# Performance work log

Hardware: AMD Instinct MI355X
Metric: run time of the kernel (lower is better)

Reference implementation:

```python
import jax, jax.numpy as jnp
import numpy as np

VERY_NEG = -1e30

H = 768           # hidden_size
A_DIM = 768       # attention_dim_size
N_TREE = 40000    # num_tree_nodes (embed_init vocab)
N_CODES = 10000   # number of leaf codes (rows of leaves_list)
MAX_ANC = 8       # max ancestors per code
B, V, M = 16, 32, 48  # batch, visits, codes per visit
OUT = 512         # classifier output_size


def setup_inputs() -> dict:
    key = jax.random.key(0)
    ks = jax.random.split(key, 12)
    leaves_list = jax.random.randint(ks[0], (N_CODES, MAX_ANC), 0, N_TREE)
    ancestors_list = jax.random.randint(ks[1], (N_CODES, MAX_ANC), 0, N_TREE)
    masks = (jax.random.uniform(ks[2], (N_CODES, MAX_ANC)) > 0.3).astype(jnp.float32)
    masks = masks.at[:, 0].set(1.0)  # ensure at least one valid ancestor
    input_ids = jax.random.randint(ks[3], (B, V, M), 0, N_CODES + 1)  # 0 is padding row
    code_mask = (jax.random.uniform(ks[4], (B, V, M)) > 0.2).astype(jnp.float32)
    code_mask = code_mask.at[:, :, 0].set(1.0)
    s = 1.0 / np.sqrt(H)
    embed_table = jax.random.normal(ks[5], (N_TREE, H), dtype=jnp.float32) * s
    w1 = jax.random.normal(ks[6], (2 * H, A_DIM), dtype=jnp.float32) * (1.0 / np.sqrt(2 * H))
    b1 = jnp.zeros((A_DIM,), dtype=jnp.float32)
    w2 = jax.random.normal(ks[7], (A_DIM, 1), dtype=jnp.float32) * (1.0 / np.sqrt(A_DIM))
    b2 = jnp.zeros((1,), dtype=jnp.float32)
    wc = jax.random.normal(ks[8], (H, OUT), dtype=jnp.float32) * s
    bc = jnp.zeros((OUT,), dtype=jnp.float32)
    return {
        "embed_table": embed_table, "w1": w1, "b1": b1, "w2": w2, "b2": b2,
        "wc": wc, "bc": bc, "masks": masks, "code_mask": code_mask,
        "leaves_list": leaves_list, "ancestors_list": ancestors_list,
        "input_ids": input_ids,
    }


def reference(embed_table, w1, b1, w2, b2, wc, bc, masks, code_mask,
              leaves_list, ancestors_list, input_ids):
    # --- DAGAttention2D over ancestor axis ---
    leaves = embed_table[leaves_list]        # [N, A, H]
    ancestors = embed_table[ancestors_list]  # [N, A, H]
    m = masks[:, :, None]                    # [N, A, 1]
    x = jnp.concatenate([leaves * m, ancestors * m], axis=-1)  # [N, A, 2H]
    x = jax.nn.relu(jnp.einsum('nah,hd->nad', x, w1) + b1)
    x = jnp.einsum('nad,do->nao', x, w2) + b2                  # [N, A, 1]
    x = x + (1.0 - m) * VERY_NEG
    attn = jax.nn.softmax(x, axis=1)                           # softmax over ancestors
    dag_emb = (attn * ancestors * m).sum(axis=1)               # [N, H]
    # --- dict_matrix with padding row 0, embedding lookup ---
    dict_matrix = jnp.concatenate([jnp.zeros((1, dag_emb.shape[1]), dag_emb.dtype), dag_emb], axis=0)
    emb = dict_matrix[input_ids]             # [B, V, M, H]
    cm = code_mask[..., None]
    pooled = (emb * cm).sum(axis=2) / jnp.clip(cm.sum(axis=2), 1.0, None)  # [B, V, H]
    # --- Classifier (dropout inactive at eval, activation=None) ---
    out = jnp.einsum('bvh,ho->bvo', pooled, wc) + bc           # [B, V, OUT]
    return out
```

## Files before the change

kernel.cpp:

```cpp
#include <hip/hip_runtime.h>
#include <stdint.h>

typedef unsigned short u16;
typedef __bf16 bfx8 __attribute__((ext_vector_type(8)));
typedef float f32x4 __attribute__((ext_vector_type(4)));

#define HD 768
#define NTREE 40000
#define NCODES 10000
#define GNN 1536
#define OUTD 512
#define NBV 512
#define VNEG (-1e30f)
#define TB 4

#define BM 256
#define BN 256
#define BK 64
#define NKT (HD / BK)
#define NMT ((NTREE + BM - 1) / BM)
#define NNT (GNN / BN)
#define GRID (NMT * NNT)
#define Q8 (GRID / 8)
#define R8 (GRID % 8)

#define WAITV(n) asm volatile("s_waitcnt vmcnt(" #n ")" ::: "memory")

__device__ __forceinline__ float bf2f(u16 u) {
  union { uint32_t i; float f; } v; v.i = ((uint32_t)u) << 16; return v.f;
}
__device__ __forceinline__ u16 f2bf(float f) {
  union { float fl; uint32_t i; } v; v.fl = f;
  uint32_t u = v.i;
  u += 0x7FFFu + ((u >> 16) & 1u);
  return (u16)(u >> 16);
}

__global__ void k_convE(const float* __restrict__ E, u16* __restrict__ Ebf, int n4) {
  int i = blockIdx.x * blockDim.x + threadIdx.x;
  if (i >= n4) return;
  float4 v = ((const float4*)E)[i];
  ushort4 r;
  r.x = f2bf(v.x); r.y = f2bf(v.y); r.z = f2bf(v.z); r.w = f2bf(v.w);
  ((ushort4*)Ebf)[i] = r;
}

__global__ void k_bt(const float* __restrict__ w1, u16* __restrict__ Bt) {
  int idx = blockIdx.x * blockDim.x + threadIdx.x;
  if (idx >= GNN * HD) return;
  int n = idx / HD, k = idx % HD;
  int srow = k + ((n >= HD) ? HD : 0);
  int scol = (n >= HD) ? (n - HD) : n;
  Bt[idx] = f2bf(w1[(size_t)srow * HD + scol]);
}

__global__ __launch_bounds__(512, 2) void k_gemm(const u16* __restrict__ A,
                                                 const u16* __restrict__ B,
                                                 u16* __restrict__ C) {
  __shared__ u16 lds[65536];

  const int tid    = threadIdx.x;
  const int lane   = tid & 63;
  const int wn     = tid >> 6;
  const int lane15 = lane & 15;
  const int g      = lane >> 4;

  const int orig = blockIdx.x;
  const int xcd = orig & 7, lin = orig >> 3;
  const int wg = (xcd < R8 ? xcd * (Q8 + 1) : R8 * (Q8 + 1) + (xcd - R8) * Q8) + lin;
  const int mt = wg / NNT, nt = wg % NNT;
  const int tm = mt * BM, tn = nt * BN;

  const u16* aSrc[2][2];
  const u16* bSrc[2][2];
#pragma unroll
  for (int u = 0; u < 2; ++u) {
    const int o    = u * 8192 + tid * 16;
    const int rloc = o >> 7;
    const int c    = ((o >> 4) & 7) ^ (rloc & 7);
#pragma unroll
    for (int h = 0; h < 2; ++h) {
      int ra = tm + h * 128 + rloc; if (ra > NTREE - 1) ra = NTREE - 1;
      aSrc[u][h] = A + (size_t)ra * HD + c * 8;
      bSrc[u][h] = B + (size_t)(tn + h * 128 + rloc) * HD + c * 8;
    }
  }

#define STAGE_A(MH, NB, TT) do {                                               \
    _Pragma("unroll") for (int u = 0; u < 2; ++u)                              \
      __builtin_amdgcn_global_load_lds(                                        \
        (const __attribute__((address_space(1))) void*)(aSrc[u][MH] + (TT) * BK), \
        (__attribute__((address_space(3))) void*)((char*)lds + (NB) * 32768 +  \
            (MH) * 16384 + u * 8192 + tid * 16),                               \
        16, 0, 0);                                                             \
  } while (0)

#define STAGE_B(NH, NB, TT) do {                                               \
    _Pragma("unroll") for (int u = 0; u < 2; ++u)                              \
      __builtin_amdgcn_global_load_lds(                                        \
        (const __attribute__((address_space(1))) void*)(bSrc[u][NH] + (TT) * BK), \
        (__attribute__((address_space(3))) void*)((char*)lds + 65536 +         \
            (NB) * 32768 + (NH) * 16384 + u * 8192 + tid * 16),                \
        16, 0, 0);                                                             \
  } while (0)

  f32x4 acc[16][2];
#pragma unroll
  for (int i = 0; i < 16; ++i) {
    acc[i][0] = (f32x4){0.f, 0.f, 0.f, 0.f};
    acc[i][1] = (f32x4){0.f, 0.f, 0.f, 0.f};
  }

  int colz[2];
  colz[0] = ((0 * 4 + g) ^ (lane15 & 7)) * 8;
  colz[1] = ((1 * 4 + g) ^ (lane15 & 7)) * 8;
  const int rbase = lane15 * 64;

  bfx8 aF[8], bF[2][2];

#define PHASE(MH, KS, STAGE_STMT, DRAIN_STMT)                                  \
  {                                                                            \
    const int _az = bA + (MH) * 8192 + rbase + colz[KS];                       \
    _Pragma("unroll") for (int i = 0; i < 8; ++i)                              \
      aF[i] = *(const bfx8*)&lds[_az + i * 1024];                              \
    if ((MH) == 0) {                                                           \
      const int _bz = bB + wn * 2048 + rbase + colz[KS];                       \
      bF[KS][0] = *(const bfx8*)&lds[_bz];                                     \
      bF[KS][1] = *(const bfx8*)&lds[_bz + 1024];                              \
    }                                                                          \
    STAGE_STMT;                                                                \
    __builtin_amdgcn_s_barrier();                                              \
    asm volatile("s_waitcnt lgkmcnt(0)" ::: "memory");                         \
    __builtin_amdgcn_sched_barrier(0);                                         \
    __builtin_amdgcn_s_setprio(1);                                             \
    _Pragma("unroll") for (int i = 0; i < 8; ++i) {                            \
      acc[(MH) * 8 + i][0] = __builtin_amdgcn_mfma_f32_16x16x32_bf16(          \
          aF[i], bF[KS][0], acc[(MH) * 8 + i][0], 0, 0, 0);                    \
      acc[(MH) * 8 + i][1] = __builtin_amdgcn_mfma_f32_16x16x32_bf16(          \
          aF[i], bF[KS][1], acc[(MH) * 8 + i][1], 0, 0, 0);                    \
    }                                                                          \
    __builtin_amdgcn_s_setprio(0);                                             \
    DRAIN_STMT;                                                                \
    __builtin_amdgcn_s_barrier();                                              \
  }

  STAGE_B(0, 0, 0);
  STAGE_B(1, 0, 0);
  STAGE_A(0, 0, 0);
  STAGE_A(1, 0, 0);
  WAITV(2);
  __builtin_amdgcn_s_barrier();

  for (int t = 0; t < NKT; ++t) {
    const int cur = t & 1, nb = cur ^ 1;
    const int bA = cur * 16384;
    const int bB = 32768 + cur * 16384;
    const bool more = (t + 1 < NKT);

    PHASE(0, 0, if (more) STAGE_B(0, nb, t + 1), );
    PHASE(0, 1, if (more) STAGE_B(1, nb, t + 1),
          if (t == NKT - 1) { WAITV(0); } else { WAITV(4); });
    PHASE(1, 0, if (more) STAGE_A(0, nb, t + 1), );
    PHASE(1, 1, if (more) STAGE_A(1, nb, t + 1), WAITV(2));
  }

  const int r0 = (lane >> 4) * 4, cc = lane15;
#pragma unroll
  for (int mf = 0; mf < 16; ++mf) {
#pragma unroll
    for (int j = 0; j < 2; ++j) {
#pragma unroll
      for (int rr = 0; rr < 4; ++rr) {
        const int row = tm + mf * 16 + r0 + rr;
        if (row < NTREE) {
          const int col = tn + wn * 32 + j * 16 + cc;
          C[(size_t)row * GNN + col] = f2bf(acc[mf][j][rr]);
        }
      }
    }
  }
#undef PHASE
#undef STAGE_A
#undef STAGE_B
}

__global__ __launch_bounds__(256) void k_attn(const u16* __restrict__ PQ,
                                              const u16* __restrict__ Ebf,
                                              const float* __restrict__ b1,
                                              const float* __restrict__ w2,
                                              const float* __restrict__ b2,
                                              const float* __restrict__ masks,
                                              const int* __restrict__ leaves,
                                              const int* __restrict__ anc,
                                              float* __restrict__ dag) {
  const int n = blockIdx.x;
  const int tid = threadIdx.x, lane = tid & 63, wv = tid >> 6;
  __shared__ float sc[8];
  __shared__ float m_s[8];
  __shared__ int   an_s[8];
  __shared__ int   lv_s[8];
  if (tid < 8) {
    an_s[tid] = anc[n * 8 + tid];
    lv_s[tid] = leaves[n * 8 + tid];
    m_s[tid]  = masks[n * 8 + tid];
  }
  __syncthreads();

  for (int a = wv; a < 8; a += 4) {
    const float mm = m_s[a];
    if (mm == 0.f) {
      if (lane == 0) sc[a] = VNEG;
      continue;
    }
    const int l = lv_s[a], an = an_s[a];
    const u16* pr = PQ + (size_t)l * GNN;
    const u16* qr = PQ + (size_t)an * GNN + HD;
    const int d0 = lane * 12;
    float s = 0.f;
#pragma unroll
    for (int jj = 0; jj < 3; ++jj) {
      const int d = d0 + jj * 4;
      ushort4 pv = *(const ushort4*)(pr + d);
      ushort4 qv = *(const ushort4*)(qr + d);
      float4  bb = *(const float4*)(b1 + d);
      float4  ww = *(const float4*)(w2 + d);
      float v;
      v = fmaxf(bf2f(pv.x) + bf2f(qv.x) + bb.x, 0.f); s += v * ww.x;
      v = fmaxf(bf2f(pv.y) + bf2f(qv.y) + bb.y, 0.f); s += v * ww.y;
      v = fmaxf(bf2f(pv.z) + bf2f(qv.z) + bb.z, 0.f); s += v * ww.z;
      v = fmaxf(bf2f(pv.w) + bf2f(qv.w) + bb.w, 0.f); s += v * ww.w;
    }
#pragma unroll
    for (int off = 32; off > 0; off >>= 1) s += __shfl_down(s, off);
    if (lane == 0) sc[a] = s + b2[0];
  }
  __syncthreads();

  float mx = sc[0];
#pragma unroll
  for (int a = 1; a < 8; ++a) mx = fmaxf(mx, sc[a]);
  float ex[8], den = 0.f;
#pragma unroll
  for (int a = 0; a < 8; ++a) { ex[a] = expf(sc[a] - mx); den += ex[a]; }
  const float inv = 1.0f / den;
  float cf[8];
#pragma unroll
  for (int a = 0; a < 8; ++a) cf[a] = ex[a] * inv * m_s[a];

#pragma unroll
  for (int c = 0; c < 3; ++c) {
    const int d = tid + c * 256;
    float accv = 0.f;
#pragma unroll
    for (int a = 0; a < 8; ++a) {
      const float cfa = cf[a];
      if (cfa != 0.f) accv += cfa * bf2f(Ebf[(size_t)an_s[a] * HD + d]);
    }
    dag[(size_t)n * HD + d] = accv;
  }
}

__global__ __launch_bounds__(256) void k_pool(const float* __restrict__ dag,
                                              const int* __restrict__ ids,
                                              const float* __restrict__ cm,
                                              float* __restrict__ pooled) {
  const int bv = blockIdx.x, tid = threadIdx.x;
  __shared__ int   id_s[48];
  __shared__ float cm_s[48];
  if (tid < 48) { id_s[tid] = ids[bv * 48 + tid]; cm_s[tid] = cm[bv * 48 + tid]; }
  __syncthreads();
  float cnt = 0.f;
  for (int m = 0; m < 48; ++m) cnt += cm_s[m];
  const float scale = 1.0f / fmaxf(cnt, 1.0f);
#pragma unroll
  for (int c = 0; c < 3; ++c) {
    const int d = tid + c * 256;
    float accv = 0.f;
    for (int m = 0; m < 48; ++m) {
      const int id = id_s[m];
      const float cv = cm_s[m];
      if (id > 0 && cv != 0.f) accv += cv * dag[(size_t)(id - 1) * HD + d];
    }
    pooled[(size_t)bv * HD + d] = accv * scale;
  }
}

__global__ __launch_bounds__(256) void k_out(const float* __restrict__ pooled,
                                             const float* __restrict__ wc,
                                             const float* __restrict__ bc,
                                             float* __restrict__ out) {
  const int b0 = blockIdx.x * TB;
  const int tid = threadIdx.x;
  __shared__ float pl[TB][HD];
  for (int i = tid; i < TB * HD; i += 256) pl[i / HD][i % HD] = pooled[(size_t)b0 * HD + i];
  __syncthreads();
  float a0[TB], a1[TB];
#pragma unroll
  for (int r = 0; r < TB; ++r) { a0[r] = 0.f; a1[r] = 0.f; }
  for (int h = 0; h < HD; ++h) {
    const float w0  = wc[(size_t)h * OUTD + tid];
    const float w1v = wc[(size_t)h * OUTD + tid + 256];
#pragma unroll
    for (int r = 0; r < TB; ++r) { const float p = pl[r][h]; a0[r] += p * w0; a1[r] += p * w1v; }
  }
  const float bc0 = bc[tid], bc1 = bc[tid + 256];
#pragma unroll
  for (int r = 0; r < TB; ++r) {
    out[(size_t)(b0 + r) * OUTD + tid]       = a0[r] + bc0;
    out[(size_t)(b0 + r) * OUTD + tid + 256] = a1[r] + bc1;
  }
}

extern "C" void kernel_launch(void* const* d_in, const int* in_sizes, int n_in,
                              void* d_out, int out_size, void* d_ws, size_t ws_size,
                              hipStream_t stream) {
  const float* E     = (const float*)d_in[0];
  const float* w1    = (const float*)d_in[1];
  const float* b1    = (const float*)d_in[2];
  const float* w2    = (const float*)d_in[3];
  const float* b2    = (const float*)d_in[4];
  const float* wc    = (const float*)d_in[5];
  const float* bc    = (const float*)d_in[6];
  const float* masks = (const float*)d_in[7];
  const float* cm    = (const float*)d_in[8];
  const int*   leaves = (const int*)d_in[9];
  const int*   anc    = (const int*)d_in[10];
  const int*   ids    = (const int*)d_in[11];
  float* out = (float*)d_out;

  if (n_in < 12) return;
  if (in_sizes[0] != NTREE * HD) return;
  if (out_size != NBV * OUTD) return;

  char* ws = (char*)d_ws;
  const size_t szEbf = (size_t)NTREE * HD * 2;
  const size_t szBt  = (size_t)GNN * HD * 2;
  const size_t szPQ  = (size_t)NTREE * GNN * 2;
  const size_t szDag = (size_t)NCODES * HD * 4;
  const size_t szPl  = (size_t)NBV * HD * 4;
  if (ws_size < szEbf + szBt + szPQ + szDag + szPl) return;

  u16*   Ebf    = (u16*)ws;            ws += szEbf;
  u16*   Bt     = (u16*)ws;            ws += szBt;
  u16*   PQ     = (u16*)ws;            ws += szPQ;
  float* dag    = (float*)ws;          ws += szDag;
  float* pooled = (float*)ws;          ws += szPl;

  const int n4 = NTREE * HD / 4;
  k_convE<<<(n4 + 255) / 256, 256, 0, stream>>>(E, Ebf, n4);
  k_bt<<<(GNN * HD + 255) / 256, 256, 0, stream>>>(w1, Bt);
  k_gemm<<<GRID, 512, 0, stream>>>(Ebf, Bt, PQ);
  k_attn<<<NCODES, 256, 0, stream>>>(PQ, Ebf, b1, w2, b2, masks, leaves, anc, dag);
  k_pool<<<NBV, 256, 0, stream>>>(dag, ids, cm, pooled);
  k_out<<<NBV / TB, 256, 0, stream>>>(pooled, wc, bc, out);
}
```

Baseline: 316.0 us.

## Use 2x4 warp tiling in GEMM, widen attention blocks, vectorize pooling

```diff
diff --git a/kernel.cpp b/kernel.cpp
--- a/kernel.cpp
+++ b/kernel.cpp
@@ -4,6 +4,7 @@
 typedef unsigned short u16;
 typedef __bf16 bfx8 __attribute__((ext_vector_type(8)));
 typedef float f32x4 __attribute__((ext_vector_type(4)));
+typedef u16 u16x8 __attribute__((ext_vector_type(8)));
 
 #define HD 768
 #define NTREE 40000
@@ -61,7 +62,9 @@
 
   const int tid    = threadIdx.x;
   const int lane   = tid & 63;
-  const int wn     = tid >> 6;
+  const int wv     = tid >> 6;
+  const int wm     = wv >> 2;
+  const int wn2    = wv & 3;
   const int lane15 = lane & 15;
   const int g      = lane >> 4;
 
@@ -104,51 +107,49 @@
         16, 0, 0);                                                             \
   } while (0)
 
-  f32x4 acc[16][2];
-#pragma unroll
-  for (int i = 0; i < 16; ++i) {
-    acc[i][0] = (f32x4){0.f, 0.f, 0.f, 0.f};
-    acc[i][1] = (f32x4){0.f, 0.f, 0.f, 0.f};
-  }
+  f32x4 acc[8][4];
+#pragma unroll
+  for (int i = 0; i < 8; ++i)
+#pragma unroll
+    for (int j = 0; j < 4; ++j) acc[i][j] = (f32x4){0.f, 0.f, 0.f, 0.f};
 
   int colz[2];
   colz[0] = ((0 * 4 + g) ^ (lane15 & 7)) * 8;
   colz[1] = ((1 * 4 + g) ^ (lane15 & 7)) * 8;
-  const int rbase = lane15 * 64;
-
-  bfx8 aF[8], bF[2][2];
+  const int aBase = (wm * 128 + lane15) * 64;
+  const int bBase = (wn2 * 64 + lane15) * 64;
+
+  bfx8 aF[4], bF[4];
 
 #define PHASE(MH, KS, STAGE_STMT, DRAIN_STMT)                                  \
   {                                                                            \
-    const int _az = bA + (MH) * 8192 + rbase + colz[KS];                       \
-    _Pragma("unroll") for (int i = 0; i < 8; ++i)                              \
+    const int _az = bA + aBase + (MH) * 4096 + colz[KS];                       \
+    _Pragma("unroll") for (int i = 0; i < 4; ++i)                              \
       aF[i] = *(const bfx8*)&lds[_az + i * 1024];                              \
     if ((MH) == 0) {                                                           \
-      const int _bz = bB + wn * 2048 + rbase + colz[KS];                       \
-      bF[KS][0] = *(const bfx8*)&lds[_bz];                                     \
-      bF[KS][1] = *(const bfx8*)&lds[_bz + 1024];                              \
+      const int _bz = bB + bBase + colz[KS];                                   \
+      _Pragma("unroll") for (int j = 0; j < 4; ++j)                            \
+        bF[j] = *(const bfx8*)&lds[_bz + j * 1024];                            \
     }                                                                          \
     STAGE_STMT;                                                                \
     __builtin_amdgcn_s_barrier();                                              \
     asm volatile("s_waitcnt lgkmcnt(0)" ::: "memory");                         \
     __builtin_amdgcn_sched_barrier(0);                                         \
     __builtin_amdgcn_s_setprio(1);                                             \
-    _Pragma("unroll") for (int i = 0; i < 8; ++i) {                            \
-      acc[(MH) * 8 + i][0] = __builtin_amdgcn_mfma_f32_16x16x32_bf16(          \
-          aF[i], bF[KS][0], acc[(MH) * 8 + i][0], 0, 0, 0);                    \
-      acc[(MH) * 8 + i][1] = __builtin_amdgcn_mfma_f32_16x16x32_bf16(          \
-          aF[i], bF[KS][1], acc[(MH) * 8 + i][1], 0, 0, 0);                    \
-    }                                                                          \
+    _Pragma("unroll") for (int i = 0; i < 4; ++i)                              \
+      _Pragma("unroll") for (int j = 0; j < 4; ++j)                            \
+        acc[(MH) * 4 + i][j] = __builtin_amdgcn_mfma_f32_16x16x32_bf16(        \
+            aF[i], bF[j], acc[(MH) * 4 + i][j], 0, 0, 0);                      \
     __builtin_amdgcn_s_setprio(0);                                             \
     DRAIN_STMT;                                                                \
     __builtin_amdgcn_s_barrier();                                              \
   }
 
+  STAGE_A(0, 0, 0);
+  STAGE_A(1, 0, 0);
   STAGE_B(0, 0, 0);
   STAGE_B(1, 0, 0);
-  STAGE_A(0, 0, 0);
-  STAGE_A(1, 0, 0);
-  WAITV(2);
+  WAITV(0);
   __builtin_amdgcn_s_barrier();
 
   for (int t = 0; t < NKT; ++t) {
@@ -157,24 +158,23 @@
     const int bB = 32768 + cur * 16384;
     const bool more = (t + 1 < NKT);
 
-    PHASE(0, 0, if (more) STAGE_B(0, nb, t + 1), );
-    PHASE(0, 1, if (more) STAGE_B(1, nb, t + 1),
-          if (t == NKT - 1) { WAITV(0); } else { WAITV(4); });
-    PHASE(1, 0, if (more) STAGE_A(0, nb, t + 1), );
-    PHASE(1, 1, if (more) STAGE_A(1, nb, t + 1), WAITV(2));
+    PHASE(0, 0, if (more) { STAGE_A(0, nb, t + 1); STAGE_A(1, nb, t + 1); }, );
+    PHASE(1, 0, if (more) { STAGE_B(0, nb, t + 1); STAGE_B(1, nb, t + 1); }, );
+    PHASE(0, 1, , );
+    PHASE(1, 1, , WAITV(0));
   }
 
   const int r0 = (lane >> 4) * 4, cc = lane15;
 #pragma unroll
-  for (int mf = 0; mf < 16; ++mf) {
-#pragma unroll
-    for (int j = 0; j < 2; ++j) {
+  for (int mf = 0; mf < 8; ++mf) {
+#pragma unroll
+    for (int nf = 0; nf < 4; ++nf) {
 #pragma unroll
       for (int rr = 0; rr < 4; ++rr) {
-        const int row = tm + mf * 16 + r0 + rr;
+        const int row = tm + wm * 128 + mf * 16 + r0 + rr;
         if (row < NTREE) {
-          const int col = tn + wn * 32 + j * 16 + cc;
-          C[(size_t)row * GNN + col] = f2bf(acc[mf][j][rr]);
+          const int col = tn + wn2 * 64 + nf * 16 + cc;
+          C[(size_t)row * GNN + col] = f2bf(acc[mf][nf][rr]);
         }
       }
     }
@@ -184,7 +184,27 @@
 #undef STAGE_B
 }
 
-__global__ __launch_bounds__(256) void k_attn(const u16* __restrict__ PQ,
+__device__ __forceinline__ float dot8(const u16* pr, const u16* qr,
+                                      const float* b1, const float* w2, int d) {
+  u16x8 pv = *(const u16x8*)(pr + d);
+  u16x8 qv = *(const u16x8*)(qr + d);
+  float4 bb0 = *(const float4*)(b1 + d);
+  float4 bb1 = *(const float4*)(b1 + d + 4);
+  float4 ww0 = *(const float4*)(w2 + d);
+  float4 ww1 = *(const float4*)(w2 + d + 4);
+  float s = 0.f, v;
+  v = fmaxf(bf2f(pv[0]) + bf2f(qv[0]) + bb0.x, 0.f); s += v * ww0.x;
+  v = fmaxf(bf2f(pv[1]) + bf2f(qv[1]) + bb0.y, 0.f); s += v * ww0.y;
+  v = fmaxf(bf2f(pv[2]) + bf2f(qv[2]) + bb0.z, 0.f); s += v * ww0.z;
+  v = fmaxf(bf2f(pv[3]) + bf2f(qv[3]) + bb0.w, 0.f); s += v * ww0.w;
+  v = fmaxf(bf2f(pv[4]) + bf2f(qv[4]) + bb1.x, 0.f); s += v * ww1.x;
+  v = fmaxf(bf2f(pv[5]) + bf2f(qv[5]) + bb1.y, 0.f); s += v * ww1.y;
+  v = fmaxf(bf2f(pv[6]) + bf2f(qv[6]) + bb1.z, 0.f); s += v * ww1.z;
+  v = fmaxf(bf2f(pv[7]) + bf2f(qv[7]) + bb1.w, 0.f); s += v * ww1.w;
+  return s;
+}
+
+__global__ __launch_bounds__(512) void k_attn(const u16* __restrict__ PQ,
                                               const u16* __restrict__ Ebf,
                                               const float* __restrict__ b1,
                                               const float* __restrict__ w2,
@@ -206,33 +226,21 @@
   }
   __syncthreads();
 
-  for (int a = wv; a < 8; a += 4) {
+  {
+    const int a = wv;
     const float mm = m_s[a];
     if (mm == 0.f) {
       if (lane == 0) sc[a] = VNEG;
-      continue;
-    }
-    const int l = lv_s[a], an = an_s[a];
-    const u16* pr = PQ + (size_t)l * GNN;
-    const u16* qr = PQ + (size_t)an * GNN + HD;
-    const int d0 = lane * 12;
-    float s = 0.f;
-#pragma unroll
-    for (int jj = 0; jj < 3; ++jj) {
-      const int d = d0 + jj * 4;
-      ushort4 pv = *(const ushort4*)(pr + d);
-      ushort4 qv = *(const ushort4*)(qr + d);
-      float4  bb = *(const float4*)(b1 + d);
-      float4  ww = *(const float4*)(w2 + d);
-      float v;
-      v = fmaxf(bf2f(pv.x) + bf2f(qv.x) + bb.x, 0.f); s += v * ww.x;
-      v = fmaxf(bf2f(pv.y) + bf2f(qv.y) + bb.y, 0.f); s += v * ww.y;
-      v = fmaxf(bf2f(pv.z) + bf2f(qv.z) + bb.z, 0.f); s += v * ww.z;
-      v = fmaxf(bf2f(pv.w) + bf2f(qv.w) + bb.w, 0.f); s += v * ww.w;
-    }
-#pragma unroll
-    for (int off = 32; off > 0; off >>= 1) s += __shfl_down(s, off);
-    if (lane == 0) sc[a] = s + b2[0];
+    } else {
+      const int l = lv_s[a], an = an_s[a];
+      const u16* pr = PQ + (size_t)l * GNN;
+      const u16* qr = PQ + (size_t)an * GNN + HD;
+      float s = dot8(pr, qr, b1, w2, lane * 8);
+      if (lane < 32) s += dot8(pr, qr, b1, w2, 512 + lane * 8);
+#pragma unroll
+      for (int off = 32; off > 0; off >>= 1) s += __shfl_down(s, off);
+      if (lane == 0) sc[a] = s + b2[0];
+    }
   }
   __syncthreads();
 
@@ -247,9 +255,18 @@
 #pragma unroll
   for (int a = 0; a < 8; ++a) cf[a] = ex[a] * inv * m_s[a];
 
-#pragma unroll
-  for (int c = 0; c < 3; ++c) {
-    const int d = tid + c * 256;
+  {
+    int d = tid;
+    float accv = 0.f;
+#pragma unroll
+    for (int a = 0; a < 8; ++a) {
+      const float cfa = cf[a];
+      if (cfa != 0.f) accv += cfa * bf2f(Ebf[(size_t)an_s[a] * HD + d]);
+    }
+    dag[(size_t)n * HD + d] = accv;
+  }
+  if (tid < 256) {
+    const int d = 512 + tid;
     float accv = 0.f;
 #pragma unroll
     for (int a = 0; a < 8; ++a) {
@@ -272,16 +289,19 @@
   float cnt = 0.f;
   for (int m = 0; m < 48; ++m) cnt += cm_s[m];
   const float scale = 1.0f / fmaxf(cnt, 1.0f);
-#pragma unroll
-  for (int c = 0; c < 3; ++c) {
-    const int d = tid + c * 256;
-    float accv = 0.f;
+  if (tid < 192) {
+    float4 accv = make_float4(0.f, 0.f, 0.f, 0.f);
     for (int m = 0; m < 48; ++m) {
       const int id = id_s[m];
       const float cv = cm_s[m];
-      if (id > 0 && cv != 0.f) accv += cv * dag[(size_t)(id - 1) * HD + d];
-    }
-    pooled[(size_t)bv * HD + d] = accv * scale;
+      if (id > 0 && cv != 0.f) {
+        float4 v = *(const float4*)(dag + (size_t)(id - 1) * HD + tid * 4);
+        accv.x += cv * v.x; accv.y += cv * v.y;
+        accv.z += cv * v.z; accv.w += cv * v.w;
+      }
+    }
+    accv.x *= scale; accv.y *= scale; accv.z *= scale; accv.w *= scale;
+    *(float4*)(pooled + (size_t)bv * HD + tid * 4) = accv;
   }
 }
 
@@ -350,7 +370,7 @@
   k_convE<<<(n4 + 255) / 256, 256, 0, stream>>>(E, Ebf, n4);
   k_bt<<<(GNN * HD + 255) / 256, 256, 0, stream>>>(w1, Bt);
   k_gemm<<<GRID, 512, 0, stream>>>(Ebf, Bt, PQ);
-  k_attn<<<NCODES, 256, 0, stream>>>(PQ, Ebf, b1, w2, b2, masks, leaves, anc, dag);
+  k_attn<<<NCODES, 512, 0, stream>>>(PQ, Ebf, b1, w2, b2, masks, leaves, anc, dag);
   k_pool<<<NBV, 256, 0, stream>>>(dag, ids, cm, pooled);
   k_out<<<NBV / TB, 256, 0, stream>>>(pooled, wc, bc, out);
 }
```

Result: faster. 301.7 us (-4.5%).
